# Kernel optimization log

Measured on AMD Instinct MI355X. Metric: run time of the kernel, lower is better.

Reference implementation:

```python
import jax, jax.numpy as jnp
import numpy as np

B, T, C = 4, 2048, 1024
N_HEAD = 16
HS = C // N_HEAD  # head_size = 64


def setup_inputs() -> dict:
    key = jax.random.key(0)
    k1, k2, k3 = jax.random.split(key, 3)
    x = jax.random.normal(k1, (B, T, C), dtype=jnp.float32)
    # torch Linear(in, out, bias=False); stored here as (in, out) so y = x @ W
    W_attn = jax.random.normal(k2, (C, 3 * C), dtype=jnp.float32) * (C ** -0.5)
    W_proj = jax.random.normal(k3, (C, C), dtype=jnp.float32) * (C ** -0.5)
    return {"x": x, "W_attn": W_attn, "W_proj": W_proj}


def reference(x, W_attn, W_proj):
    Bq, Tq, Cq = x.shape
    qkv = x @ W_attn                              # (B, T, 3C)
    q, k, v = jnp.split(qkv, 3, axis=-1)          # each (B, T, C)
    # (B, T, C) -> (B, H, T, hs)
    q = q.reshape(Bq, Tq, N_HEAD, HS).transpose(0, 2, 1, 3)
    k = k.reshape(Bq, Tq, N_HEAD, HS).transpose(0, 2, 1, 3)
    v = v.reshape(Bq, Tq, N_HEAD, HS).transpose(0, 2, 1, 3)
    scale = HS ** -0.5
    att = jnp.einsum("bhqd,bhkd->bhqk", q, k) * scale  # (B, H, T, T)
    causal = jnp.tril(jnp.ones((Tq, Tq), dtype=bool))
    att = jnp.where(causal[None, None], att, jnp.finfo(att.dtype).min)
    att = jax.nn.softmax(att, axis=-1)
    y = jnp.einsum("bhqk,bhkd->bhqd", att, v)     # (B, H, T, hs)
    y = y.transpose(0, 2, 1, 3).reshape(Bq, Tq, Cq)
    return y @ W_proj                             # (B, T, C)
```

## Files before the change

kernel.cpp:

```cpp
#include <hip/hip_runtime.h>
#include <stdint.h>

typedef __bf16 bf16x8 __attribute__((ext_vector_type(8)));
typedef float f32x4 __attribute__((ext_vector_type(4)));

__device__ __forceinline__ unsigned short f2bf(float f) {
  unsigned u = __builtin_bit_cast(unsigned, f);
  u = (u + 0x7fffu + ((u >> 16) & 1u)) >> 16;
  return (unsigned short)u;
}

__device__ __forceinline__ unsigned cvt_pk_bf16(float a, float b) {
  unsigned r;
  asm("v_cvt_pk_bf16_f32 %0, %1, %2" : "=v"(r) : "v"(a), "v"(b));
  return r;
}

__device__ __forceinline__ void gload_lds16(const unsigned short* g, unsigned short* l) {
  __builtin_amdgcn_global_load_lds(
      (__attribute__((address_space(1))) unsigned int*)g,
      (__attribute__((address_space(3))) unsigned int*)l, 16, 0, 0);
}

__device__ __forceinline__ void store_val(float* p, float v) { *p = v; }
__device__ __forceinline__ void store_val(unsigned short* p, float v) { *p = f2bf(v); }

__global__ __launch_bounds__(256) void f2bf_kernel(const float* __restrict__ in,
                                                   unsigned short* __restrict__ out, int n) {
  int stride = gridDim.x * blockDim.x * 4;
  for (int i = (blockIdx.x * blockDim.x + threadIdx.x) * 4; i < n; i += stride) {
    float4 v = *(const float4*)(in + i);
    ushort4 o;
    o.x = f2bf(v.x); o.y = f2bf(v.y); o.z = f2bf(v.z); o.w = f2bf(v.w);
    *(ushort4*)(out + i) = o;
  }
}

__global__ __launch_bounds__(256) void transpose_f2bf(const float* __restrict__ in,
                                                      unsigned short* __restrict__ out,
                                                      int R, int Ccols, float qscale, int qcols) {
  __shared__ unsigned short t[64][65];
  int r0 = blockIdx.y * 64, c0 = blockIdx.x * 64;
  int tid = threadIdx.x;
#pragma unroll
  for (int rep = 0; rep < 16; rep++) {
    int idx = rep * 256 + tid;
    int rr = idx >> 6, cc = idx & 63;
    float v = in[(size_t)(r0 + rr) * Ccols + c0 + cc];
    if (c0 + cc < qcols) v *= qscale;
    t[rr][cc] = f2bf(v);
  }
  __syncthreads();
#pragma unroll
  for (int rep = 0; rep < 16; rep++) {
    int idx = rep * 256 + tid;
    int cc = idx >> 6, rr = idx & 63;
    out[(size_t)(c0 + cc) * R + r0 + rr] = t[rr][cc];
  }
}

template <typename OutT, bool WRITEV>
__global__ __launch_bounds__(512, 2) void gemm_bt(const unsigned short* __restrict__ A,
                                                  const unsigned short* __restrict__ Bt,
                                                  OutT* __restrict__ C, int M, int N, int K,
                                                  int mtiles, unsigned short* __restrict__ vt) {
  __shared__ unsigned short lds3[3][24576];
  const int tid = threadIdx.x;
  const int wid = tid >> 6, l = tid & 63;
  const int wm = wid >> 2, wn = wid & 3;
  const int lr = l & 15, lg = l >> 4;

  int nwg = gridDim.x;
  int q8 = nwg >> 3;
  int bid = blockIdx.x;
  int bs = (bid & 7) * q8 + (bid >> 3);
  int mt = bs % mtiles, nt = bs / mtiles;
  const int m0 = mt * 128, n0 = nt * 256;

  const int srow = tid >> 3;
  const int schunk = ((tid & 7) ^ (srow & 7)) * 8;
  const unsigned short* gA0 = A + (size_t)(m0 + srow) * K + schunk;
  const unsigned short* gB0 = Bt + (size_t)(n0 + srow) * K + schunk;
  const int wslice = wid * 512;

  int arow[4], brow[2][2], xoff[2];
#pragma unroll
  for (int m = 0; m < 4; m++) arow[m] = (wm * 64 + m * 16 + lr) * 64;
#pragma unroll
  for (int qq = 0; qq < 2; qq++)
#pragma unroll
    for (int j = 0; j < 2; j++) brow[qq][j] = 8192 + (wn * 64 + qq * 32 + j * 16 + lr) * 64;
#pragma unroll
  for (int ks = 0; ks < 2; ks++) xoff[ks] = ((ks * 4 + lg) ^ (lr & 7)) * 8;

  f32x4 acc[4][4] = {};
  const int NT = K >> 6;

  gload_lds16(gA0, &lds3[0][wslice]);
  gload_lds16(gA0 + (size_t)64 * K, &lds3[0][4096 + wslice]);
#pragma unroll
  for (int u = 0; u < 4; u++)
    gload_lds16(gB0 + (size_t)(u * 64) * K, &lds3[0][8192 + u * 4096 + wslice]);
  gload_lds16(gA0 + 64, &lds3[1][wslice]);
  gload_lds16(gA0 + (size_t)64 * K + 64, &lds3[1][4096 + wslice]);
#pragma unroll
  for (int u = 0; u < 4; u++)
    gload_lds16(gB0 + (size_t)(u * 64) * K + 64, &lds3[1][8192 + u * 4096 + wslice]);

  int cb = 0;
  for (int t = 0; t < NT; t++) {
    if (t == NT - 1) {
      asm volatile("s_waitcnt vmcnt(0)" ::: "memory");
    } else {
      asm volatile("s_waitcnt vmcnt(6)" ::: "memory");
    }
    __builtin_amdgcn_s_barrier();
    const unsigned short* bufc = lds3[cb];
    int pb = cb + 2; if (pb >= 3) pb -= 3;
    unsigned short* bufp = lds3[pb];
    const int k2 = (t + 2) * 64;
    const bool pre = (t + 2) < NT;

    if (pre) {
      gload_lds16(gA0 + k2, bufp + wslice);
      gload_lds16(gA0 + (size_t)64 * K + k2, bufp + 4096 + wslice);
      gload_lds16(gB0 + k2, bufp + 8192 + wslice);
    }
    bf16x8 af[4][2];
#pragma unroll
    for (int m = 0; m < 4; m++)
#pragma unroll
      for (int ks = 0; ks < 2; ks++)
        af[m][ks] = *(const bf16x8*)&bufc[arow[m] + xoff[ks]];
    {
      bf16x8 bq[2][2];
#pragma unroll
      for (int j = 0; j < 2; j++)
#pragma unroll
        for (int ks = 0; ks < 2; ks++)
          bq[j][ks] = *(const bf16x8*)&bufc[brow[0][j] + xoff[ks]];
      __builtin_amdgcn_s_setprio(1);
#pragma unroll
      for (int m = 0; m < 4; m++)
#pragma unroll
        for (int j = 0; j < 2; j++)
#pragma unroll
          for (int ks = 0; ks < 2; ks++)
            acc[m][j] = __builtin_amdgcn_mfma_f32_16x16x32_bf16(af[m][ks], bq[j][ks], acc[m][j], 0, 0, 0);
      __builtin_amdgcn_s_setprio(0);
    }
    if (pre) {
      gload_lds16(gB0 + (size_t)64 * K + k2, bufp + 12288 + wslice);
      gload_lds16(gB0 + (size_t)128 * K + k2, bufp + 16384 + wslice);
      gload_lds16(gB0 + (size_t)192 * K + k2, bufp + 20480 + wslice);
    }
    {
      bf16x8 bq[2][2];
#pragma unroll
      for (int j = 0; j < 2; j++)
#pragma unroll
        for (int ks = 0; ks < 2; ks++)
          bq[j][ks] = *(const bf16x8*)&bufc[brow[1][j] + xoff[ks]];
      __builtin_amdgcn_s_setprio(1);
#pragma unroll
      for (int m = 0; m < 4; m++)
#pragma unroll
        for (int j = 0; j < 2; j++)
#pragma unroll
          for (int ks = 0; ks < 2; ks++)
            acc[m][2 + j] = __builtin_amdgcn_mfma_f32_16x16x32_bf16(af[m][ks], bq[j][ks], acc[m][2 + j], 0, 0, 0);
      __builtin_amdgcn_s_setprio(0);
    }
    cb = (cb == 2) ? 0 : cb + 1;
  }

  if (WRITEV && n0 >= 2048) {
    int hh = ((n0 - 2048) >> 6) + wn;
#pragma unroll
    for (int m = 0; m < 4; m++) {
      int row = m0 + wm * 64 + m * 16 + lg * 4;
      int bb = row >> 11, tt = row & 2047;
      size_t base = (size_t)(bb * 16 + hh) * 131072 + tt;
#pragma unroll
      for (int n = 0; n < 4; n++) {
        int d = n * 16 + lr;
        ushort4 v;
        v.x = f2bf(acc[m][n][0]); v.y = f2bf(acc[m][n][1]);
        v.z = f2bf(acc[m][n][2]); v.w = f2bf(acc[m][n][3]);
        *(ushort4*)&vt[base + (size_t)d * 2048] = v;
      }
    }
  } else {
#pragma unroll
    for (int m = 0; m < 4; m++)
#pragma unroll
      for (int n = 0; n < 4; n++)
#pragma unroll
        for (int i = 0; i < 4; i++) {
          size_t row = (size_t)(m0 + wm * 64 + m * 16 + lg * 4 + i);
          size_t col = (size_t)(n0 + wn * 64 + n * 16 + lr);
          store_val(&C[row * N + col], acc[m][n][i]);
        }
  }
}

__global__ __launch_bounds__(256, 3) void attn_kernel(const unsigned short* __restrict__ qkv,
                                                      const unsigned short* __restrict__ vt,
                                                      unsigned short* __restrict__ y) {
  __shared__ unsigned short k_lds[2][64 * 64];
  __shared__ unsigned short v_lds[2][64 * 64];
  __shared__ unsigned short p_lds[8][16 * 64];
  int tid = threadIdx.x;
  int w = tid >> 6, l = tid & 63;
  int lr = l & 15, lg = l >> 4;
  int g4 = lg * 4;
  int lband = l & 48;
  int bh = blockIdx.x;
  int b = bh >> 4, h = bh & 15;
  int qgrp = 15 - blockIdx.y;
  int q0 = qgrp * 128 + w * 32;

  char* plo = (char*)p_lds[w * 2];
  char* phi = (char*)p_lds[w * 2 + 1];

  int srow = tid >> 3;
  int schunk = (tid & 7) ^ (srow & 7);
  const unsigned short* gK0 = qkv + (size_t)(b * 2048 + srow) * 3072 + 1024 + h * 64 + schunk * 8;
  const unsigned short* gK1 = gK0 + (size_t)32 * 3072;
  const unsigned short* gV0 = vt + (size_t)bh * 131072 + (size_t)srow * 2048 + schunk * 8;
  const unsigned short* gV1 = gV0 + (size_t)32 * 2048;
  int ldsbase0 = w * 512;
  int ldsbase1 = 2048 + w * 512;

  const unsigned short* qp = qkv + (size_t)(b * 2048 + q0 + lr) * 3072 + h * 64 + lg * 8;
  bf16x8 aQ0lo = *(const bf16x8*)qp;
  bf16x8 aQ1lo = *(const bf16x8*)(qp + 32);
  bf16x8 aQ0hi = *(const bf16x8*)(qp + 16 * 3072);
  bf16x8 aQ1hi = *(const bf16x8*)(qp + 16 * 3072 + 32);

  f32x4 Olo[4] = {}, Ohi[4] = {};
  float sumlo = 0.f, sumhi = 0.f;

  int rx = lr & 7;
  int kc0 = (lg ^ rx) * 8;
  int kc1 = ((4 + lg) ^ rx) * 8;

  int nbmax = ((qgrp * 128 + 96) >> 6) + 1;
  int kend = q0 + 31;
  int kdiag = q0 >> 6;

  gload_lds16(gK0, &k_lds[0][ldsbase0]);
  gload_lds16(gK1, &k_lds[0][ldsbase1]);
  gload_lds16(gV0, &v_lds[0][ldsbase0]);
  gload_lds16(gV1, &v_lds[0][ldsbase1]);

  int cur = 0;
  for (int kb = 0; kb < nbmax; kb++) {
    int kbase = kb * 64;
    if (kb + 1 < nbmax) {
      size_t koff = (size_t)(kbase + 64) * 3072;
      size_t voff = (size_t)(kbase + 64);
      int nxt = cur ^ 1;
      gload_lds16(gK0 + koff, &k_lds[nxt][ldsbase0]);
      gload_lds16(gK1 + koff, &k_lds[nxt][ldsbase1]);
      gload_lds16(gV0 + voff, &v_lds[nxt][ldsbase0]);
      gload_lds16(gV1 + voff, &v_lds[nxt][ldsbase1]);
      asm volatile("s_waitcnt vmcnt(4)" ::: "memory");
    } else {
      asm volatile("s_waitcnt vmcnt(0)" ::: "memory");
    }
    __builtin_amdgcn_s_barrier();
    if (kbase <= kend) {
      const unsigned short* kl = k_lds[cur];
      const unsigned short* vl = v_lds[cur];
      f32x4 svlo[4], svhi[4];
      __builtin_amdgcn_s_setprio(1);
#pragma unroll
      for (int n = 0; n < 4; n++) {
        bf16x8 kf0 = *(const bf16x8*)&kl[(n * 16 + lr) * 64 + kc0];
        bf16x8 kf1 = *(const bf16x8*)&kl[(n * 16 + lr) * 64 + kc1];
        f32x4 z = {};
        z = __builtin_amdgcn_mfma_f32_16x16x32_bf16(kf0, aQ0lo, z, 0, 0, 0);
        z = __builtin_amdgcn_mfma_f32_16x16x32_bf16(kf1, aQ1lo, z, 0, 0, 0);
        svlo[n] = z;
        f32x4 z2 = {};
        z2 = __builtin_amdgcn_mfma_f32_16x16x32_bf16(kf0, aQ0hi, z2, 0, 0, 0);
        z2 = __builtin_amdgcn_mfma_f32_16x16x32_bf16(kf1, aQ1hi, z2, 0, 0, 0);
        svhi[n] = z2;
      }
      __builtin_amdgcn_s_setprio(0);
      if (kb == kdiag) {
#pragma unroll
        for (int n = 0; n < 4; n++)
#pragma unroll
          for (int i = 0; i < 4; i++) {
            int kk = kbase + n * 16 + g4 + i;
            if (kk > q0 + lr) svlo[n][i] = -1.0e38f;
            if (kk > q0 + 16 + lr) svhi[n][i] = -1.0e38f;
          }
      }
      float pslo = 0.f, pshi = 0.f;
      unsigned pk0lo[4], pk1lo[4], pk0hi[4], pk1hi[4];
#pragma unroll
      for (int n = 0; n < 4; n++) {
        float a0 = __builtin_amdgcn_exp2f(svlo[n][0]);
        float a1 = __builtin_amdgcn_exp2f(svlo[n][1]);
        float a2 = __builtin_amdgcn_exp2f(svlo[n][2]);
        float a3 = __builtin_amdgcn_exp2f(svlo[n][3]);
        pslo += (a0 + a1) + (a2 + a3);
        pk0lo[n] = cvt_pk_bf16(a0, a1);
        pk1lo[n] = cvt_pk_bf16(a2, a3);
        float c0 = __builtin_amdgcn_exp2f(svhi[n][0]);
        float c1 = __builtin_amdgcn_exp2f(svhi[n][1]);
        float c2 = __builtin_amdgcn_exp2f(svhi[n][2]);
        float c3 = __builtin_amdgcn_exp2f(svhi[n][3]);
        pshi += (c0 + c1) + (c2 + c3);
        pk0hi[n] = cvt_pk_bf16(c0, c1);
        pk1hi[n] = cvt_pk_bf16(c2, c3);
      }
      pslo += __shfl_xor(pslo, 16);
      pslo += __shfl_xor(pslo, 32);
      pshi += __shfl_xor(pshi, 16);
      pshi += __shfl_xor(pshi, 32);
      sumlo += pslo;
      sumhi += pshi;
#pragma unroll
      for (int n = 0; n < 4; n++) {
        int chunk = (2 * n + (lg >> 1)) ^ rx;
        int off = lr * 128 + chunk * 16 + (lg & 1) * 8;
        *(uint2*)(plo + off) = make_uint2(pk0lo[n], pk1lo[n]);
        *(uint2*)(phi + off) = make_uint2(pk0hi[n], pk1hi[n]);
      }
      bf16x8 aPlo0 = *(const bf16x8*)(plo + lr * 128 + (lg ^ rx) * 16);
      bf16x8 aPlo1 = *(const bf16x8*)(plo + lr * 128 + ((4 + lg) ^ rx) * 16);
      bf16x8 aPhi0 = *(const bf16x8*)(phi + lr * 128 + (lg ^ rx) * 16);
      bf16x8 aPhi1 = *(const bf16x8*)(phi + lr * 128 + ((4 + lg) ^ rx) * 16);
      __builtin_amdgcn_s_setprio(1);
#pragma unroll
      for (int n2 = 0; n2 < 4; n2++) {
        bf16x8 v0 = *(const bf16x8*)&vl[(n2 * 16 + lr) * 64 + kc0];
        bf16x8 v1 = *(const bf16x8*)&vl[(n2 * 16 + lr) * 64 + kc1];
        Olo[n2] = __builtin_amdgcn_mfma_f32_16x16x32_bf16(aPlo0, v0, Olo[n2], 0, 0, 0);
        Olo[n2] = __builtin_amdgcn_mfma_f32_16x16x32_bf16(aPlo1, v1, Olo[n2], 0, 0, 0);
        Ohi[n2] = __builtin_amdgcn_mfma_f32_16x16x32_bf16(aPhi0, v0, Ohi[n2], 0, 0, 0);
        Ohi[n2] = __builtin_amdgcn_mfma_f32_16x16x32_bf16(aPhi1, v1, Ohi[n2], 0, 0, 0);
      }
      __builtin_amdgcn_s_setprio(0);
    }
    __builtin_amdgcn_s_barrier();
    cur ^= 1;
  }
  float s0 = __shfl(sumlo, lband | g4);
  float s1 = __shfl(sumlo, lband | (g4 + 1));
  float s2 = __shfl(sumlo, lband | (g4 + 2));
  float s3 = __shfl(sumlo, lband | (g4 + 3));
  float t0 = __shfl(sumhi, lband | g4);
  float t1 = __shfl(sumhi, lband | (g4 + 1));
  float t2 = __shfl(sumhi, lband | (g4 + 2));
  float t3 = __shfl(sumhi, lband | (g4 + 3));
  float rl0 = 1.f / s0, rl1 = 1.f / s1, rl2 = 1.f / s2, rl3 = 1.f / s3;
  float rh0 = 1.f / t0, rh1 = 1.f / t1, rh2 = 1.f / t2, rh3 = 1.f / t3;
#pragma unroll
  for (int n2 = 0; n2 < 4; n2++) {
    size_t base = (size_t)(b * 2048 + q0 + g4) * 1024 + h * 64 + n2 * 16 + lr;
    y[base] = f2bf(Olo[n2][0] * rl0);
    y[base + 1024] = f2bf(Olo[n2][1] * rl1);
    y[base + 2048] = f2bf(Olo[n2][2] * rl2);
    y[base + 3072] = f2bf(Olo[n2][3] * rl3);
    size_t bhh = base + (size_t)16 * 1024;
    y[bhh] = f2bf(Ohi[n2][0] * rh0);
    y[bhh + 1024] = f2bf(Ohi[n2][1] * rh1);
    y[bhh + 2048] = f2bf(Ohi[n2][2] * rh2);
    y[bhh + 3072] = f2bf(Ohi[n2][3] * rh3);
  }
}

extern "C" void kernel_launch(void* const* d_in, const int* in_sizes, int n_in,
                              void* d_out, int out_size, void* d_ws, size_t ws_size,
                              hipStream_t stream) {
  const float* x = (const float*)d_in[0];
  const float* Wa = (const float*)d_in[1];
  const float* Wp = (const float*)d_in[2];
  float* out = (float*)d_out;

  char* ws = (char*)d_ws;
  size_t off = 0;
  unsigned short* xb = (unsigned short*)(ws + off);   off += (size_t)8192 * 1024 * 2;
  unsigned short* Wta = (unsigned short*)(ws + off);  off += (size_t)3072 * 1024 * 2;
  unsigned short* Wtp = (unsigned short*)(ws + off);  off += (size_t)1024 * 1024 * 2;
  unsigned short* qkvb = (unsigned short*)(ws + off); off += (size_t)8192 * 3072 * 2;
  unsigned short* vtb = (unsigned short*)(ws + off);  off += (size_t)64 * 64 * 2048 * 2;
  unsigned short* yb = (unsigned short*)(ws + off);   off += (size_t)8192 * 1024 * 2;

  const float SC = 0.125f * 1.44269504f;
  f2bf_kernel<<<2048, 256, 0, stream>>>(x, xb, 8192 * 1024);
  transpose_f2bf<<<dim3(48, 16), 256, 0, stream>>>(Wa, Wta, 1024, 3072, SC, 1024);
  transpose_f2bf<<<dim3(16, 16), 256, 0, stream>>>(Wp, Wtp, 1024, 1024, 1.0f, 0);
  gemm_bt<unsigned short, true><<<768, 512, 0, stream>>>(xb, Wta, qkvb, 8192, 3072, 1024, 64, vtb);
  attn_kernel<<<dim3(64, 16), 256, 0, stream>>>(qkvb, vtb, yb);
  gemm_bt<float, false><<<256, 512, 0, stream>>>(yb, Wtp, out, 8192, 1024, 1024, 64, nullptr);
}
```

Measured before the change: 161.3 us.

## Add dedicated QKV GEMM kernel with 128x192 tiles and double buffering

Replaces the templated QKV GEMM (128x256 tiles, triple-buffered LDS, 768 workgroups) with a specialized kernel using 128x192 tiles, a two-stage LDS double buffer of about 80KB, and launch bounds allowing more resident workgroups. The grid becomes 1024 workgroups, which divides more evenly across the CUs. The V-transpose epilogue is now handled per 16-column fragment. In exchange, each tile reuses operands less and the shallower pipeline leaves less room to hide load latency.

```diff
diff --git a/kernel.cpp b/kernel.cpp
--- a/kernel.cpp
+++ b/kernel.cpp
@@ -59,11 +59,113 @@
   }
 }
 
-template <typename OutT, bool WRITEV>
+__global__ __launch_bounds__(512, 4) void gemm_qkv(const unsigned short* __restrict__ A,
+                                                   const unsigned short* __restrict__ Bt,
+                                                   unsigned short* __restrict__ C,
+                                                   unsigned short* __restrict__ vt) {
+  const int K = 1024, N = 3072, NT = 16, MT = 64;
+  __shared__ unsigned short lds[2][20480];
+  const int tid = threadIdx.x;
+  const int wid = tid >> 6, l = tid & 63;
+  const int wm = wid >> 2, wn = wid & 3;
+  const int lr = l & 15, lg = l >> 4;
+
+  int nwg = gridDim.x;
+  int q8 = nwg >> 3;
+  int bid = blockIdx.x;
+  int bs = (bid & 7) * q8 + (bid >> 3);
+  int mt = bs % MT, nt = bs / MT;
+  const int m0 = mt * 128, n0 = nt * 192;
+
+  const int srow = tid >> 3;
+  const int schunk = ((tid & 7) ^ (srow & 7)) * 8;
+  const unsigned short* gA0 = A + (size_t)(m0 + srow) * K + schunk;
+  const unsigned short* gB0 = Bt + (size_t)(n0 + srow) * K + schunk;
+  const int dst = tid * 8;
+
+  int arow[4], brow[3], xoff[2];
+#pragma unroll
+  for (int m = 0; m < 4; m++) arow[m] = (wm * 64 + m * 16 + lr) * 64;
+#pragma unroll
+  for (int n = 0; n < 3; n++) brow[n] = 8192 + (wn * 48 + n * 16 + lr) * 64;
+#pragma unroll
+  for (int ks = 0; ks < 2; ks++) xoff[ks] = ((ks * 4 + lg) ^ (lr & 7)) * 8;
+
+  f32x4 acc[4][3] = {};
+
+  gload_lds16(gA0, &lds[0][dst]);
+  gload_lds16(gA0 + (size_t)64 * K, &lds[0][4096 + dst]);
+  gload_lds16(gB0, &lds[0][8192 + dst]);
+  gload_lds16(gB0 + (size_t)64 * K, &lds[0][12288 + dst]);
+  gload_lds16(gB0 + (size_t)128 * K, &lds[0][16384 + dst]);
+
+  int cur = 0;
+  for (int t = 0; t < NT; t++) {
+    if (t + 1 < NT) {
+      int k1 = (t + 1) * 64;
+      unsigned short* bp = lds[cur ^ 1];
+      gload_lds16(gA0 + k1, bp + dst);
+      gload_lds16(gA0 + (size_t)64 * K + k1, bp + 4096 + dst);
+      gload_lds16(gB0 + k1, bp + 8192 + dst);
+      gload_lds16(gB0 + (size_t)64 * K + k1, bp + 12288 + dst);
+      gload_lds16(gB0 + (size_t)128 * K + k1, bp + 16384 + dst);
+      asm volatile("s_waitcnt vmcnt(5)" ::: "memory");
+    } else {
+      asm volatile("s_waitcnt vmcnt(0)" ::: "memory");
+    }
+    __builtin_amdgcn_s_barrier();
+    const unsigned short* bufc = lds[cur];
+    bf16x8 af[4][2], bq[3][2];
+#pragma unroll
+    for (int m = 0; m < 4; m++)
+#pragma unroll
+      for (int ks = 0; ks < 2; ks++)
+        af[m][ks] = *(const bf16x8*)&bufc[arow[m] + xoff[ks]];
+#pragma unroll
+    for (int n = 0; n < 3; n++)
+#pragma unroll
+      for (int ks = 0; ks < 2; ks++)
+        bq[n][ks] = *(const bf16x8*)&bufc[brow[n] + xoff[ks]];
+    __builtin_amdgcn_s_setprio(1);
+#pragma unroll
+    for (int m = 0; m < 4; m++)
+#pragma unroll
+      for (int n = 0; n < 3; n++)
+#pragma unroll
+        for (int ks = 0; ks < 2; ks++)
+          acc[m][n] = __builtin_amdgcn_mfma_f32_16x16x32_bf16(af[m][ks], bq[n][ks], acc[m][n], 0, 0, 0);
+    __builtin_amdgcn_s_setprio(0);
+    __builtin_amdgcn_s_barrier();
+    cur ^= 1;
+  }
+
+#pragma unroll
+  for (int m = 0; m < 4; m++) {
+    int row = m0 + wm * 64 + m * 16 + lg * 4;
+#pragma unroll
+    for (int n = 0; n < 3; n++) {
+      int cb = n0 + wn * 48 + n * 16;
+      if (cb >= 2048) {
+        int h = (cb - 2048) >> 6;
+        int d = ((cb - 2048) & 63) + lr;
+        int bb = row >> 11, tt = row & 2047;
+        ushort4 v;
+        v.x = f2bf(acc[m][n][0]); v.y = f2bf(acc[m][n][1]);
+        v.z = f2bf(acc[m][n][2]); v.w = f2bf(acc[m][n][3]);
+        *(ushort4*)&vt[(size_t)(bb * 16 + h) * 131072 + (size_t)d * 2048 + tt] = v;
+      } else {
+#pragma unroll
+        for (int i = 0; i < 4; i++)
+          C[(size_t)(row + i) * N + cb + lr] = f2bf(acc[m][n][i]);
+      }
+    }
+  }
+}
+
 __global__ __launch_bounds__(512, 2) void gemm_bt(const unsigned short* __restrict__ A,
                                                   const unsigned short* __restrict__ Bt,
-                                                  OutT* __restrict__ C, int M, int N, int K,
-                                                  int mtiles, unsigned short* __restrict__ vt) {
+                                                  float* __restrict__ C, int M, int N, int K,
+                                                  int mtiles) {
   __shared__ unsigned short lds3[3][24576];
   const int tid = threadIdx.x;
   const int wid = tid >> 6, l = tid & 63;
@@ -174,34 +276,16 @@
     cb = (cb == 2) ? 0 : cb + 1;
   }
 
-  if (WRITEV && n0 >= 2048) {
-    int hh = ((n0 - 2048) >> 6) + wn;
-#pragma unroll
-    for (int m = 0; m < 4; m++) {
-      int row = m0 + wm * 64 + m * 16 + lg * 4;
-      int bb = row >> 11, tt = row & 2047;
-      size_t base = (size_t)(bb * 16 + hh) * 131072 + tt;
-#pragma unroll
-      for (int n = 0; n < 4; n++) {
-        int d = n * 16 + lr;
-        ushort4 v;
-        v.x = f2bf(acc[m][n][0]); v.y = f2bf(acc[m][n][1]);
-        v.z = f2bf(acc[m][n][2]); v.w = f2bf(acc[m][n][3]);
-        *(ushort4*)&vt[base + (size_t)d * 2048] = v;
-      }
-    }
-  } else {
-#pragma unroll
-    for (int m = 0; m < 4; m++)
-#pragma unroll
-      for (int n = 0; n < 4; n++)
-#pragma unroll
-        for (int i = 0; i < 4; i++) {
-          size_t row = (size_t)(m0 + wm * 64 + m * 16 + lg * 4 + i);
-          size_t col = (size_t)(n0 + wn * 64 + n * 16 + lr);
-          store_val(&C[row * N + col], acc[m][n][i]);
-        }
-  }
+#pragma unroll
+  for (int m = 0; m < 4; m++)
+#pragma unroll
+    for (int n = 0; n < 4; n++)
+#pragma unroll
+      for (int i = 0; i < 4; i++) {
+        size_t row = (size_t)(m0 + wm * 64 + m * 16 + lg * 4 + i);
+        size_t col = (size_t)(n0 + wn * 64 + n * 16 + lr);
+        C[row * N + col] = acc[m][n][i];
+      }
 }
 
 __global__ __launch_bounds__(256, 3) void attn_kernel(const unsigned short* __restrict__ qkv,
@@ -396,7 +480,7 @@
   f2bf_kernel<<<2048, 256, 0, stream>>>(x, xb, 8192 * 1024);
   transpose_f2bf<<<dim3(48, 16), 256, 0, stream>>>(Wa, Wta, 1024, 3072, SC, 1024);
   transpose_f2bf<<<dim3(16, 16), 256, 0, stream>>>(Wp, Wtp, 1024, 1024, 1.0f, 0);
-  gemm_bt<unsigned short, true><<<768, 512, 0, stream>>>(xb, Wta, qkvb, 8192, 3072, 1024, 64, vtb);
+  gemm_qkv<<<1024, 512, 0, stream>>>(xb, Wta, qkvb, vtb);
   attn_kernel<<<dim3(64, 16), 256, 0, stream>>>(qkvb, vtb, yb);
-  gemm_bt<float, false><<<256, 512, 0, stream>>>(yb, Wtp, out, 8192, 1024, 1024, 64, nullptr);
-}
+  gemm_bt<<<256, 512, 0, stream>>>(yb, Wtp, out, 8192, 1024, 1024, 64);
+}
```

Result: no change. 163.3 us (+1.2%).
